# Performance work log

Hardware: AMD Instinct MI355X
Metric: run time of the kernel (lower is better)

Reference implementation:

```python
import jax, jax.numpy as jnp
import numpy as np

CUTOFF = 0.05

def _freq_filter(x_chw, filter_type):
    # x_chw: [C,H,W] = batch element 0, detached in the original (stop_gradient)
    x = jax.lax.stop_gradient(x_chw)
    C, H, W = x.shape
    a = jnp.abs(x)
    mn = a.min(axis=(1, 2), keepdims=True)
    ptp = a.max(axis=(1, 2), keepdims=True) - mn
    # np.uint8(255*(a-mn)/ptp): values in [0,255], cast truncates -> floor
    q = jnp.floor(255.0 * (a - mn) / ptp)
    f = jnp.fft.fftshift(jnp.fft.fft2(q), axes=(-2, -1))
    crow, ccol = H // 2, W // 2
    dr, dc = int(CUTOFF * crow), int(CUTOFF * ccol)
    m = jnp.zeros((H, W), dtype=q.dtype)
    m = m.at[crow - dr:crow + dr, ccol - dc:ccol + dc].set(1.0)
    if filter_type == 'low_pass':
        m = 1.0 - m  # note: original 'low_pass' actually removes low freqs
    out = jnp.abs(jnp.fft.ifft2(jnp.fft.ifftshift(f * m, axes=(-2, -1))))
    return out.astype(x_chw.dtype)  # [C,H,W]

def _conv1x1(x, w, b):
    # x: [B,C,H,W], w: [O,C], b: [O]
    return jnp.einsum('oc,bchw->bohw', w, x) + b[None, :, None, None]

def setup_inputs() -> dict:
    key = jax.random.key(0)
    ks = jax.random.split(key, 7)
    B, C, H, W = 1, 256, 96, 96
    fuse = jax.random.normal(ks[0], (B, C, H, W), dtype=jnp.float32)
    s = 1.0 / np.sqrt(C)
    Wq = jax.random.normal(ks[1], (C, C), dtype=jnp.float32) * s
    bq = jax.random.normal(ks[2], (C,), dtype=jnp.float32) * 0.01
    Wk = jax.random.normal(ks[3], (C, C), dtype=jnp.float32) * s
    bk = jax.random.normal(ks[4], (C,), dtype=jnp.float32) * 0.01
    Wv = jax.random.normal(ks[5], (C, C), dtype=jnp.float32) * s
    bv = jax.random.normal(ks[6], (C,), dtype=jnp.float32) * 0.01
    return {"fuse": fuse, "Wq": Wq, "bq": bq, "Wk": Wk, "bk": bk, "Wv": Wv, "bv": bv}

def reference(fuse, Wq, bq, Wk, bk, Wv, bv):
    B, C, H, W = fuse.shape
    scale = 1.0 / (C ** 0.5)
    # frequency-filtered maps (computed from batch 0, broadcast to all batches)
    FQ = jnp.broadcast_to(_freq_filter(fuse[0], 'high_pass'), fuse.shape)
    FK = jnp.broadcast_to(_freq_filter(fuse[0], 'low_pass'), fuse.shape)
    fuse_Query = _conv1x1(FQ, Wq, bq).reshape(B, C, H * W)     # [B,C,HW]
    fuse_Q_mask = fuse_Query.reshape(B * H, C * W)             # [B*H, C*W]
    fuse_Query_t = jnp.transpose(fuse_Query, (0, 2, 1))        # [B,HW,C]
    fuse_Key = _conv1x1(FK, Wk, bk).reshape(B, C, H * W)       # [B,C,HW]
    Fuse_Q_mask = jnp.max(fuse_Q_mask, axis=0, keepdims=True)  # [1, C*W]
    mask_KQ = jnp.einsum('bnc,bcm->bnm', fuse_Query_t, fuse_Key) * scale  # [B,HW,HW]
    mask_KQ = jax.nn.softmax(mask_KQ, axis=0)  # softmax over batch dim (as in original)
    mask_KQ = jnp.max(mask_KQ, axis=1)                         # [B,HW]
    mask_KQ = mask_KQ.reshape(-1, W)                           # [B*H, W]
    mask_KQ = jnp.max(mask_KQ, axis=-1, keepdims=True)         # [B*H, 1]
    mask = (mask_KQ @ Fuse_Q_mask).reshape(B, C, H, W)
    fuse_Value = _conv1x1(fuse, Wv, bv)
    return fuse_Value + fuse_Value * mask
```

## Files before the change

### kernel.cpp

```cpp
#include <hip/hip_runtime.h>
#include <math.h>

#define CCH 256
#define HW  9216
#define CW  24576
#define TWO_PI 6.28318530717958647692f

typedef __attribute__((ext_vector_type(8))) short short8;
typedef __attribute__((ext_vector_type(4))) float f32x4;

__device__ inline unsigned short f2bf(float f) {
    unsigned u = __float_as_uint(f);
    unsigned r = (u + 0x7FFFu + ((u >> 16) & 1u)) >> 16;
    return (unsigned short)r;
}

__global__ __launch_bounds__(768) void k_pre(const float* __restrict__ x,
                                             const float* __restrict__ Wq,
                                             const float* __restrict__ Wv,
                                             short8* __restrict__ Wqt,
                                             short8* __restrict__ Wvt,
                                             unsigned* __restrict__ FQm,
                                             float* __restrict__ Fg) {
    __shared__ float qa[HW];
    __shared__ float cs[96][2];
    __shared__ float Gp[8][96][5];
    __shared__ float Gs[96][6];
    __shared__ float red[24];
    __shared__ float s_mn, s_ptp;
    int bid = blockIdx.x, t = threadIdx.x;

    if (bid >= 256) {
        int widx = bid - 256;
        if (t < 256) {
            const float* src = (widx >= 32) ? Wv : Wq;
            short8* dst = (widx >= 32) ? Wvt : Wqt;
            int cidx = (widx & 31) * 256 + t;
            int ot = cidx >> 11, kc = (cidx >> 6) & 31, m = cidx & 63;
            const float* s = src + (ot * 64 + m) * 256 + kc * 8;
            short8 v;
            #pragma unroll
            for (int e = 0; e < 8; ++e) v[e] = (short)f2bf(s[e]);
            dst[cidx] = v;
        }
        return;
    }

    int c = bid;
    if (t < 96) FQm[c * 96 + t] = 0u;
    const float* xp = x + c * HW;
    if (t < 96) { float a = TWO_PI * (float)t / 96.0f; cs[t][0] = cosf(a); cs[t][1] = sinf(a); }
    float lo = 1e30f, hi = 0.f;
    #pragma unroll
    for (int i = 0; i < 12; ++i) {
        float a = fabsf(xp[t + i * 768]);
        qa[t + i * 768] = a;
        lo = fminf(lo, a);
        hi = fmaxf(hi, a);
    }
    #pragma unroll
    for (int d = 32; d; d >>= 1) {
        lo = fminf(lo, __shfl_xor(lo, d, 64));
        hi = fmaxf(hi, __shfl_xor(hi, d, 64));
    }
    if ((t & 63) == 0) { red[t >> 6] = lo; red[12 + (t >> 6)] = hi; }
    __syncthreads();
    if (t == 0) {
        lo = red[0]; hi = red[12];
        #pragma unroll
        for (int i = 1; i < 12; ++i) { lo = fminf(lo, red[i]); hi = fmaxf(hi, red[12 + i]); }
        s_mn = lo; s_ptp = hi - lo;
    }
    __syncthreads();
    float mn = s_mn, ptp = s_ptp;

    {
        int xx = t % 96, h = t / 96;
        float g0r = 0, g0i = 0, g1r = 0, g1i = 0, g2 = 0;
        for (int y = h * 12; y < h * 12 + 12; ++y) {
            float q = floorf(255.0f * (qa[y * 96 + xx] - mn) / ptp);
            float c1 = cs[y][0], s1 = cs[y][1];
            float c2 = c1 * c1 - s1 * s1, s2 = 2.0f * c1 * s1;
            g0r += q * c2; g0i += q * s2;
            g1r += q * c1; g1i += q * s1;
            g2  += q;
        }
        Gp[h][xx][0] = g0r; Gp[h][xx][1] = g0i;
        Gp[h][xx][2] = g1r; Gp[h][xx][3] = g1i;
        Gp[h][xx][4] = g2;
    }
    __syncthreads();
    if (t < 96) {
        #pragma unroll
        for (int j = 0; j < 5; ++j) {
            float s = 0.f;
            #pragma unroll
            for (int h = 0; h < 8; ++h) s += Gp[h][t][j];
            Gs[t][j] = s;
        }
        Gs[t][5] = 0.f;
    }
    __syncthreads();
    if (t < 64) {
        int coef = t >> 2, qq = t & 3;
        int ky = coef >> 2, kx = coef & 3;
        float fr = 0, fi = 0;
        for (int xx = qq * 24; xx < qq * 24 + 24; ++xx) {
            float c1 = cs[xx][0], s1 = cs[xx][1];
            float er, ei;
            if (kx == 0)      { er = c1 * c1 - s1 * s1; ei = 2.0f * c1 * s1; }
            else if (kx == 1) { er = c1; ei = s1; }
            else if (kx == 2) { er = 1.f; ei = 0.f; }
            else              { er = c1; ei = -s1; }
            float gr, gi;
            if (ky == 0)      { gr = Gs[xx][0]; gi = Gs[xx][1]; }
            else if (ky == 1) { gr = Gs[xx][2]; gi = Gs[xx][3]; }
            else if (ky == 2) { gr = Gs[xx][4]; gi = 0.f; }
            else              { gr = Gs[xx][2]; gi = -Gs[xx][3]; }
            fr += gr * er - gi * ei;
            fi += gr * ei + gi * er;
        }
        fr += __shfl_xor(fr, 1, 64); fr += __shfl_xor(fr, 2, 64);
        fi += __shfl_xor(fi, 1, 64); fi += __shfl_xor(fi, 2, 64);
        if (qq == 0) {
            Fg[c * 32 + 2 * coef]     = fr;
            Fg[c * 32 + 2 * coef + 1] = fi;
        }
    }
}

__global__ __launch_bounds__(512) void k_gemmQ(const short8* __restrict__ Wqt,
                                               const float* __restrict__ Fg,
                                               const float* __restrict__ bq,
                                               unsigned* __restrict__ FQm) {
    __shared__ short8 As[2048];
    __shared__ short8 Bs[2048];
    __shared__ float Rs[2048][2];
    float (*fq)[64] = (float (*)[64])Rs;
    float (*Ts)[9]  = (float (*)[9])As;
    int tid = threadIdx.x;
    int pt_ = blockIdx.x;
    int p0 = pt_ * 64;

    int l = tid & 63, w = tid >> 6;
    int rw = w >> 2, cw = w & 3;
    int l15 = l & 15, quad = l >> 4;
    int abase = rw * 32 + l15;
    int bbase = cw * 16 + l15;

    short8 areg[4];
    #pragma unroll
    for (int i = 0; i < 4; ++i) areg[i] = Wqt[i * 512 + tid];

    int y0 = p0 / 96;
    if (tid < 64) {
        int xx = (p0 + tid) % 96;
        float axv = TWO_PI * (float)xx / 96.0f;
        float cxv = cosf(axv), sxv = sinf(axv);
        float cx2 = cxv * cxv - sxv * sxv, sx2 = 2.f * cxv * sxv;
        Ts[tid][0] = cx2;  Ts[tid][1] = cxv;  Ts[tid][2] = 1.f; Ts[tid][3] = cxv;
        Ts[tid][4] = -sx2; Ts[tid][5] = -sxv; Ts[tid][6] = 0.f; Ts[tid][7] = sxv;
    }
    {
        int yi = (tid >> 2) & 1, kx = tid & 3, cb = tid >> 3;
        float ay = TWO_PI * (float)(y0 + yi) / 96.0f;
        float cyv = cosf(ay), syv = sinf(ay);
        float cy2 = cyv * cyv - syv * syv, sy2 = 2.f * cyv * syv;
        float Ur[4] = { cy2, cyv, 1.f, cyv };
        float Ui[4] = { -sy2, -syv, 0.f, syv };
        #pragma unroll
        for (int i = 0; i < 4; ++i) {
            int cc = cb + i * 64;
            float rr = 0.f, ri = 0.f;
            #pragma unroll
            for (int ky = 0; ky < 4; ++ky) {
                float fr = Fg[cc * 32 + 2 * (ky * 4 + kx)];
                float fi = Fg[cc * 32 + 2 * (ky * 4 + kx) + 1];
                rr += fr * Ur[ky] - fi * Ui[ky];
                ri += fr * Ui[ky] + fi * Ur[ky];
            }
            Rs[cc * 8 + yi * 4 + kx][0] = rr;
            Rs[cc * 8 + yi * 4 + kx][1] = ri;
        }
    }
    __syncthreads();
    const float inv = 1.0f / 9216.0f;
    #pragma unroll
    for (int i = 0; i < 4; ++i) {
        int si = i * 512 + tid;
        int kcg = si >> 6, n = si & 63;
        int p = p0 + n;
        int y = p / 96;
        int yi = y - y0;
        float Tr[4], Ti[4];
        #pragma unroll
        for (int j = 0; j < 4; ++j) { Tr[j] = Ts[n][j]; Ti[j] = Ts[n][4 + j]; }
        short8 vv;
        #pragma unroll
        for (int e = 0; e < 8; ++e) {
            int rb = (kcg * 8 + e) * 8 + yi * 4;
            float ar = 0.f, ai = 0.f;
            #pragma unroll
            for (int kx = 0; kx < 4; ++kx) {
                float rr = Rs[rb + kx][0], ri = Rs[rb + kx][1];
                ar += rr * Tr[kx] - ri * Ti[kx];
                ai += rr * Ti[kx] + ri * Tr[kx];
            }
            vv[e] = (short)f2bf(sqrtf(ar * ar + ai * ai) * inv);
        }
        Bs[si] = vv;
    }
    __syncthreads();

    float vmax[4];
    #pragma unroll
    for (int r = 0; r < 4; ++r) vmax[r] = -3.0e38f;

    #pragma unroll
    for (int ot = 0; ot < 4; ++ot) {
        #pragma unroll
        for (int i = 0; i < 4; ++i) As[i * 512 + tid] = areg[i];
        __syncthreads();
        if (ot < 3) {
            #pragma unroll
            for (int i = 0; i < 4; ++i) areg[i] = Wqt[(ot + 1) * 2048 + i * 512 + tid];
        }
        f32x4 acc[2] = {};
        #pragma unroll
        for (int s = 0; s < 8; ++s) {
            int kc = s * 4 + quad;
            short8 a0 = As[kc * 64 + abase];
            short8 a1 = As[kc * 64 + abase + 16];
            short8 b0 = Bs[kc * 64 + bbase];
            acc[0] = __builtin_amdgcn_mfma_f32_16x16x32_bf16(a0, b0, acc[0], 0, 0, 0);
            acc[1] = __builtin_amdgcn_mfma_f32_16x16x32_bf16(a1, b0, acc[1], 0, 0, 0);
        }
        #pragma unroll
        for (int r = 0; r < 4; ++r) {
            int o_lo = ot * 64 + rw * 32 + quad * 4 + r;
            float v = fmaxf(acc[0][r] + bq[o_lo], acc[1][r] + bq[o_lo + 16]);
            vmax[r] = fmaxf(vmax[r], v);
        }
        __syncthreads();
    }

    #pragma unroll
    for (int r = 0; r < 4; ++r)
        vmax[r] = fmaxf(vmax[r], __shfl_xor(vmax[r], 32, 64));
    if (rw == 0 && quad < 2) {
        #pragma unroll
        for (int r = 0; r < 4; ++r)
            fq[quad * 4 + r][cw * 16 + l15] = vmax[r];
    }
    __syncthreads();
    if (rw == 1 && quad < 2) {
        #pragma unroll
        for (int r = 0; r < 4; ++r) {
            int row = quad * 4 + r;
            int col = cw * 16 + l15;
            float v = fmaxf(vmax[r], fq[row][col]);
            int p = p0 + col;
            int k = row * HW + p;
            if (k >= CW) k -= CW;
            if (k >= CW) k -= CW;
            unsigned u = __float_as_uint(v);
            unsigned key = (u & 0x80000000u) ? ~u : (u | 0x80000000u);
            atomicMax(&FQm[k], key);
        }
    }
}

__device__ inline float mdecode(unsigned key) {
    unsigned ub = (key & 0x80000000u) ? (key ^ 0x80000000u) : ~key;
    return __uint_as_float(ub);
}
__global__ __launch_bounds__(512) void k_gemmV(const short8* __restrict__ Wvt,
                                               const float* __restrict__ bv,
                                               const float* __restrict__ x,
                                               const unsigned* __restrict__ FQm,
                                               float* __restrict__ out) {
    __shared__ short8 As[2048];
    __shared__ short8 Bs[2048];
    int tid = threadIdx.x;
    int pt_ = blockIdx.x;
    int yv = blockIdx.y;
    int p0 = pt_ * 64;

    int l = tid & 63, w = tid >> 6;
    int rw = w >> 2, cw = w & 3;
    int l15 = l & 15, quad = l >> 4;
    int abase = rw * 32 + l15;
    int bbase = cw * 16 + l15;

    short8 areg[4];
    #pragma unroll
    for (int i = 0; i < 4; ++i) areg[i] = Wvt[(yv * 2) * 2048 + i * 512 + tid];

    #pragma unroll
    for (int i = 0; i < 4; ++i) {
        int si = i * 512 + tid;
        int KC = si >> 6, n = si & 63;
        const float* xb = x + (size_t)(KC * 8) * HW + p0 + n;
        short8 v;
        #pragma unroll
        for (int e = 0; e < 8; ++e) v[e] = (short)f2bf(xb[(size_t)e * HW]);
        Bs[si] = v;
    }

    float msk[4];
    #pragma unroll
    for (int r = 0; r < 4; ++r) {
        int row = (quad * 4 + r) & 7;
        int p = p0 + cw * 16 + l15;
        int k = row * HW + p;
        if (k >= CW) k -= CW;
        if (k >= CW) k -= CW;
        msk[r] = mdecode(FQm[k]);
    }

    #pragma unroll
    for (int j = 0; j < 2; ++j) {
        int ot = yv * 2 + j;
        #pragma unroll
        for (int i = 0; i < 4; ++i) As[i * 512 + tid] = areg[i];
        __syncthreads();
        if (j == 0) {
            #pragma unroll
            for (int i = 0; i < 4; ++i) areg[i] = Wvt[(yv * 2 + 1) * 2048 + i * 512 + tid];
        }
        f32x4 acc[2] = {};
        #pragma unroll
        for (int s = 0; s < 8; ++s) {
            int kc = s * 4 + quad;
            short8 a0 = As[kc * 64 + abase];
            short8 a1 = As[kc * 64 + abase + 16];
            short8 b0 = Bs[kc * 64 + bbase];
            acc[0] = __builtin_amdgcn_mfma_f32_16x16x32_bf16(a0, b0, acc[0], 0, 0, 0);
            acc[1] = __builtin_amdgcn_mfma_f32_16x16x32_bf16(a1, b0, acc[1], 0, 0, 0);
        }
        #pragma unroll
        for (int mi = 0; mi < 2; ++mi) {
            #pragma unroll
            for (int r = 0; r < 4; ++r) {
                int o = ot * 64 + rw * 32 + mi * 16 + quad * 4 + r;
                int p = p0 + cw * 16 + l15;
                out[(size_t)o * HW + p] = (acc[mi][r] + bv[o]) * (1.0f + msk[r]);
            }
        }
        __syncthreads();
    }
}

extern "C" void kernel_launch(void* const* d_in, const int* in_sizes, int n_in,
                              void* d_out, int out_size, void* d_ws, size_t ws_size,
                              hipStream_t stream) {
    const float* fuse = (const float*)d_in[0];
    const float* Wq   = (const float*)d_in[1];
    const float* bq   = (const float*)d_in[2];
    const float* Wv   = (const float*)d_in[5];
    const float* bv   = (const float*)d_in[6];
    float* out = (float*)d_out;

    char* ws = (char*)d_ws;
    unsigned* FQm = (unsigned*)(ws);
    float*    Fg  = (float*)(ws + 98304);
    short8*   Wqt = (short8*)(ws + 131072);
    short8*   Wvt = (short8*)(ws + 262144);

    k_pre<<<320, 768, 0, stream>>>(fuse, Wq, Wv, Wqt, Wvt, FQm, Fg);
    k_gemmQ<<<144, 512, 0, stream>>>(Wqt, Fg, bq, FQm);
    k_gemmV<<<dim3(144, 2), 512, 0, stream>>>(Wvt, bv, fuse, FQm, out);
}
```

Before: 100.9 us.

## Split Q GEMM column tiles in half and vectorize abs/minmax loads

The Q-projection kernel now gives each block 32 pixel columns instead of 64 and launches 288 blocks instead of 144, so more CUs are busy. The warp layout becomes 4x2 with one MFMA accumulator per wave, and the cross-wave max reduction is reworked to combine four partial rows through shared memory. Separately, the preprocessing kernel reads the input with float4 loads when computing abs, min and max. The trade-off is that each block reloads the full Wq matrix and recomputes the twiddle factors, so weight traffic and redundant setup work double.

```diff
diff --git a/kernel.cpp b/kernel.cpp
--- a/kernel.cpp
+++ b/kernel.cpp
@@ -51,12 +51,17 @@
     const float* xp = x + c * HW;
     if (t < 96) { float a = TWO_PI * (float)t / 96.0f; cs[t][0] = cosf(a); cs[t][1] = sinf(a); }
     float lo = 1e30f, hi = 0.f;
-    #pragma unroll
-    for (int i = 0; i < 12; ++i) {
-        float a = fabsf(xp[t + i * 768]);
-        qa[t + i * 768] = a;
-        lo = fminf(lo, a);
-        hi = fmaxf(hi, a);
+    {
+        const float4* xp4 = (const float4*)xp;
+        float4* qa4 = (float4*)qa;
+        #pragma unroll
+        for (int i = 0; i < 3; ++i) {
+            float4 v = xp4[t + i * 768];
+            v.x = fabsf(v.x); v.y = fabsf(v.y); v.z = fabsf(v.z); v.w = fabsf(v.w);
+            qa4[t + i * 768] = v;
+            lo = fminf(lo, fminf(fminf(v.x, v.y), fminf(v.z, v.w)));
+            hi = fmaxf(hi, fmaxf(fmaxf(v.x, v.y), fmaxf(v.z, v.w)));
+        }
     }
     #pragma unroll
     for (int d = 32; d; d >>= 1) {
@@ -134,27 +139,29 @@
                                                const float* __restrict__ bq,
                                                unsigned* __restrict__ FQm) {
     __shared__ short8 As[2048];
-    __shared__ short8 Bs[2048];
+    __shared__ short8 Bs[1024];
     __shared__ float Rs[2048][2];
-    float (*fq)[64] = (float (*)[64])Rs;
-    float (*Ts)[9]  = (float (*)[9])As;
+    float (*fq)[8][32] = (float (*)[8][32])Rs;
+    float (*Ts)[9]     = (float (*)[9])As;
     int tid = threadIdx.x;
-    int pt_ = blockIdx.x;
-    int p0 = pt_ * 64;
+    int pt2 = blockIdx.x;
+    int pt_ = pt2 >> 1, half = pt2 & 1;
+    int p0  = pt_ * 64;
+    int pc0 = p0 + half * 32;
 
     int l = tid & 63, w = tid >> 6;
-    int rw = w >> 2, cw = w & 3;
+    int mb = w >> 1, nb = w & 1;
     int l15 = l & 15, quad = l >> 4;
-    int abase = rw * 32 + l15;
-    int bbase = cw * 16 + l15;
+    int abase = mb * 16 + l15;
+    int bbase = nb * 16 + l15;
 
     short8 areg[4];
     #pragma unroll
     for (int i = 0; i < 4; ++i) areg[i] = Wqt[i * 512 + tid];
 
     int y0 = p0 / 96;
-    if (tid < 64) {
-        int xx = (p0 + tid) % 96;
+    if (tid < 32) {
+        int xx = (pc0 + tid) % 96;
         float axv = TWO_PI * (float)xx / 96.0f;
         float cxv = cosf(axv), sxv = sinf(axv);
         float cx2 = cxv * cxv - sxv * sxv, sx2 = 2.f * cxv * sxv;
@@ -186,10 +193,10 @@
     __syncthreads();
     const float inv = 1.0f / 9216.0f;
     #pragma unroll
-    for (int i = 0; i < 4; ++i) {
+    for (int i = 0; i < 2; ++i) {
         int si = i * 512 + tid;
-        int kcg = si >> 6, n = si & 63;
-        int p = p0 + n;
+        int kcg = si >> 5, n = si & 31;
+        int p = pc0 + n;
         int y = p / 96;
         int yi = y - y0;
         float Tr[4], Ti[4];
@@ -225,21 +232,18 @@
             #pragma unroll
             for (int i = 0; i < 4; ++i) areg[i] = Wqt[(ot + 1) * 2048 + i * 512 + tid];
         }
-        f32x4 acc[2] = {};
+        f32x4 acc = {};
         #pragma unroll
         for (int s = 0; s < 8; ++s) {
             int kc = s * 4 + quad;
             short8 a0 = As[kc * 64 + abase];
-            short8 a1 = As[kc * 64 + abase + 16];
-            short8 b0 = Bs[kc * 64 + bbase];
-            acc[0] = __builtin_amdgcn_mfma_f32_16x16x32_bf16(a0, b0, acc[0], 0, 0, 0);
-            acc[1] = __builtin_amdgcn_mfma_f32_16x16x32_bf16(a1, b0, acc[1], 0, 0, 0);
+            short8 b0 = Bs[kc * 32 + bbase];
+            acc = __builtin_amdgcn_mfma_f32_16x16x32_bf16(a0, b0, acc, 0, 0, 0);
         }
         #pragma unroll
         for (int r = 0; r < 4; ++r) {
-            int o_lo = ot * 64 + rw * 32 + quad * 4 + r;
-            float v = fmaxf(acc[0][r] + bq[o_lo], acc[1][r] + bq[o_lo + 16]);
-            vmax[r] = fmaxf(vmax[r], v);
+            int o = ot * 64 + mb * 16 + quad * 4 + r;
+            vmax[r] = fmaxf(vmax[r], acc[r] + bq[o]);
         }
         __syncthreads();
     }
@@ -247,20 +251,20 @@
     #pragma unroll
     for (int r = 0; r < 4; ++r)
         vmax[r] = fmaxf(vmax[r], __shfl_xor(vmax[r], 32, 64));
-    if (rw == 0 && quad < 2) {
+    if (quad < 2) {
         #pragma unroll
         for (int r = 0; r < 4; ++r)
-            fq[quad * 4 + r][cw * 16 + l15] = vmax[r];
-    }
-    __syncthreads();
-    if (rw == 1 && quad < 2) {
+            fq[mb][quad * 4 + r][nb * 16 + l15] = vmax[r];
+    }
+    __syncthreads();
+    if (w < 2 && quad < 2) {
         #pragma unroll
         for (int r = 0; r < 4; ++r) {
-            int row = quad * 4 + r;
-            int col = cw * 16 + l15;
-            float v = fmaxf(vmax[r], fq[row][col]);
-            int p = p0 + col;
-            int k = row * HW + p;
+            int cls = quad * 4 + r;
+            int col = nb * 16 + l15;
+            float v = fmaxf(fmaxf(fq[0][cls][col], fq[1][cls][col]),
+                            fmaxf(fq[2][cls][col], fq[3][cls][col]));
+            int k = cls * HW + pc0 + col;
             if (k >= CW) k -= CW;
             if (k >= CW) k -= CW;
             unsigned u = __float_as_uint(v);
@@ -368,6 +372,6 @@
     short8*   Wvt = (short8*)(ws + 262144);
 
     k_pre<<<320, 768, 0, stream>>>(fuse, Wq, Wv, Wqt, Wvt, FQm, Fg);
-    k_gemmQ<<<144, 512, 0, stream>>>(Wqt, Fg, bq, FQm);
+    k_gemmQ<<<288, 512, 0, stream>>>(Wqt, Fg, bq, FQm);
     k_gemmV<<<dim3(144, 2), 512, 0, stream>>>(Wvt, bv, fuse, FQm, out);
 }
```

Measured after the change: 102.5 us. Within noise of the previous version (+1.6%).
